# Kernel tuning notes

Measured on AMD Instinct MI355X. Metric: run time of the kernel, lower is better.

Reference implementation:

```python
import jax, jax.numpy as jnp
import numpy as np

D_MODEL = 768
D_INNER = 1536   # expand=2
D_STATE = 16
D_CONV = 4
DT_RANK = 48     # ceil(768/16)
B, T, N = 2, 4, 196


def _rmsnorm(x, w, eps=1e-5):
    var = jnp.mean(x * x, axis=-1, keepdims=True)
    return x * jax.lax.rsqrt(var + eps) * w


def _causal_dwconv(x, w, b):
    # x: (b, l, di), w: (di, k) depthwise, causal left-pad k-1
    xc = jnp.swapaxes(x, 1, 2)  # (b, di, l)
    out = jax.lax.conv_general_dilated(
        xc, w[:, None, :], window_strides=(1,), padding=[(D_CONV - 1, 0)],
        feature_group_count=D_INNER, dimension_numbers=('NCH', 'OIH', 'NCH'))
    return jnp.swapaxes(out + b[None, :, None], 1, 2)


def _selective_scan(u, dt, A, Bm, Cm, Dp):
    # u, dt: (b,l,di); Bm, Cm: (b,l,n); A: (di,n); Dp: (di,)
    dA = jnp.exp(dt[..., None] * A)                    # (b,l,di,n)
    dBu = (dt * u)[..., None] * Bm[:, :, None, :]      # (b,l,di,n)

    def step(h, inp):
        dA_t, dBu_t, C_t = inp
        h = dA_t * h + dBu_t                           # (b,di,n)
        return h, jnp.einsum('bdn,bn->bd', h, C_t)

    h0 = jnp.zeros((u.shape[0], D_INNER, D_STATE), u.dtype)
    _, ys = jax.lax.scan(step, h0, (jnp.swapaxes(dA, 0, 1),
                                    jnp.swapaxes(dBu, 0, 1),
                                    jnp.swapaxes(Cm, 0, 1)))
    return jnp.swapaxes(ys, 0, 1) + u * Dp


def _mamba(x, in_w, cw, cb, xp_w, dt_w, dt_b, A_log, Dp, out_w):
    xz = jnp.einsum('blc,ec->ble', x, in_w)            # (b,l,2*di)
    xb, z = jnp.split(xz, 2, axis=-1)
    xb = jax.nn.silu(_causal_dwconv(xb, cw, cb))
    x_dbl = jnp.einsum('bld,ed->ble', xb, xp_w)        # (b,l,dt_rank+2n)
    dt, Bm, Cm = jnp.split(x_dbl, [DT_RANK, DT_RANK + D_STATE], axis=-1)
    dt = jax.nn.softplus(jnp.einsum('blr,dr->bld', dt, dt_w) + dt_b)
    y = _selective_scan(xb, dt, -jnp.exp(A_log), Bm, Cm, Dp)
    y = y * jax.nn.silu(z)
    return jnp.einsum('bld,cd->blc', y, out_w)


def _block(x, i, norm_w, in_proj_w, conv_w, conv_b, x_proj_w, dt_proj_w,
           dt_proj_b, A_log, D, mix_out_w):
    # residual Mamba block: x + mixer(norm(x)); zero-initialized ssm/conv state
    return x + _mamba(_rmsnorm(x, norm_w[i]), in_proj_w[i], conv_w[i], conv_b[i],
                      x_proj_w[i], dt_proj_w[i], dt_proj_b[i], A_log[i], D[i],
                      mix_out_w[i])


def _bimamba(x, norm_w, in_proj_w, conv_w, conv_b, x_proj_w, dt_proj_w,
             dt_proj_b, A_log, D, mix_out_w, gate_w, gate_b, proj_w, proj_b):
    b, t, n, c = x.shape
    xs = x.reshape(b, t * n, c)
    params = (norm_w, in_proj_w, conv_w, conv_b, x_proj_w, dt_proj_w,
              dt_proj_b, A_log, D, mix_out_w)
    out_f = _block(xs, 0, *params)
    flip_t = lambda y: y.reshape(b, t, n, c)[:, ::-1].reshape(b, t * n, c)
    out_b = flip_t(_block(flip_t(xs), 1, *params))
    gate = jax.nn.sigmoid(
        jnp.einsum('blc,dc->bld', jnp.concatenate([out_f, out_b], -1), gate_w)
        + gate_b)
    out = gate * out_f + (1.0 - gate) * out_b
    out = jnp.einsum('bld,cd->blc', out, proj_w) + proj_b
    return out.reshape(b, t, n, c)


def setup_inputs() -> dict:
    key = jax.random.key(0)
    ks = jax.random.split(key, 12)
    s = 0.02
    a_log = jnp.broadcast_to(
        jnp.log(jnp.arange(1, D_STATE + 1, dtype=jnp.float32)),
        (2, D_INNER, D_STATE)).copy()
    return {
        'x': jax.random.normal(ks[0], (B, T, N, D_MODEL), jnp.float32),
        'norm_w': jnp.ones((2, D_MODEL), jnp.float32),
        'in_proj_w': jax.random.normal(ks[1], (2, 2 * D_INNER, D_MODEL), jnp.float32) * s,
        'conv_w': jax.random.normal(ks[2], (2, D_INNER, D_CONV), jnp.float32) * 0.2,
        'conv_b': jnp.zeros((2, D_INNER), jnp.float32),
        'x_proj_w': jax.random.normal(ks[3], (2, DT_RANK + 2 * D_STATE, D_INNER), jnp.float32) * s,
        'dt_proj_w': jax.random.normal(ks[4], (2, D_INNER, DT_RANK), jnp.float32) * s,
        'dt_proj_b': jax.random.normal(ks[5], (2, D_INNER), jnp.float32) * 0.5 - 4.0,
        'A_log': a_log,
        'D': jnp.ones((2, D_INNER), jnp.float32),
        'mix_out_w': jax.random.normal(ks[6], (2, D_MODEL, D_INNER), jnp.float32) * s,
        'gate_w': jax.random.normal(ks[7], (D_MODEL, 2 * D_MODEL), jnp.float32) * s,
        'gate_b': jnp.zeros((D_MODEL,), jnp.float32),
        'proj_w': jax.random.normal(ks[8], (D_MODEL, D_MODEL), jnp.float32) * s,
        'proj_b': jnp.zeros((D_MODEL,), jnp.float32),
    }


def reference(x, norm_w, in_proj_w, conv_w, conv_b, x_proj_w, dt_proj_w,
              dt_proj_b, A_log, D, mix_out_w, gate_w, gate_b, proj_w, proj_b):
    return _bimamba(x, norm_w, in_proj_w, conv_w, conv_b, x_proj_w, dt_proj_w,
                    dt_proj_b, A_log, D, mix_out_w, gate_w, gate_b, proj_w,
                    proj_b)
```

## Files before the change

### kernel.cpp

```cpp
#include <hip/hip_runtime.h>
#include <cstdint>
#include <cstddef>

#define BB 2
#define TT 4
#define NN 196
#define LL (TT*NN)
#define BLr (BB*LL)
#define CM 768
#define DI 1536
#define DS 16
#define DTR 48
#define XD 80
#define GCH 16
#define LC (LL/GCH)
#define NST (2*BB*DI*DS)

typedef short s16x8 __attribute__((ext_vector_type(8)));
typedef float f32x4 __attribute__((ext_vector_type(4)));

static __device__ __forceinline__ float sigmoidf_(float x) {
  return 1.f / (1.f + __expf(-x));
}
static __device__ __forceinline__ unsigned short f2bf(float f) {
  unsigned int u = __float_as_uint(f);
  unsigned int r = (u + 0x7fffu + ((u >> 16) & 1u)) >> 16;
  return (unsigned short)r;
}
static __device__ __forceinline__ float bf2f(unsigned short u) {
  return __uint_as_float(((unsigned int)u) << 16);
}
static __device__ __forceinline__ float softplusf_(float v) {
  return (v > 20.f) ? v : __logf(1.f + __expf(v));
}
static __device__ __forceinline__ void gload_lds16(const void* g, void* l) {
  __builtin_amdgcn_global_load_lds(
      (const __attribute__((address_space(1))) void*)g,
      (__attribute__((address_space(3))) void*)l, 16, 0, 0);
}

__global__ __launch_bounds__(256) void rmsnorm_k(const float* __restrict__ x,
    const float* __restrict__ nw, unsigned short* __restrict__ xn)
{
  int blk = blockIdx.x;
  int l   = blk % LL;
  int b   = (blk / LL) % BB;
  int dir = blk / (BB*LL);
  int lsrc = l;
  if (dir == 1) { int t = l / NN, n = l % NN; lsrc = (TT-1-t)*NN + n; }
  const float* xp = x + ((size_t)b*LL + lsrc)*CM;
  float s = 0.f;
  for (int c = threadIdx.x; c < CM; c += 256) { float v = xp[c]; s += v*v; }
  #pragma unroll
  for (int off = 32; off > 0; off >>= 1) s += __shfl_down(s, off);
  __shared__ float red[4];
  if ((threadIdx.x & 63) == 0) red[threadIdx.x >> 6] = s;
  __syncthreads();
  float tot = red[0] + red[1] + red[2] + red[3];
  float r = rsqrtf(tot * (1.f/CM) + 1e-5f);
  const float* w = nw + dir*CM;
  unsigned short* o = xn + (size_t)blk*CM;
  for (int c = threadIdx.x; c < CM; c += 256) o[c] = f2bf(xp[c] * r * w[c]);
}

#define S_INW  4718592
#define S_OUTW 2359296
#define S_GATW 1179648
#define S_PRJW 589824
#define S_XPW  245760
#define S_DTW  196608
#define E0 S_INW
#define E1 (E0 + S_OUTW)
#define E2 (E1 + S_GATW)
#define E3 (E2 + S_PRJW)
#define E4 (E3 + S_XPW)
#define E5 (E4 + S_DTW)
__global__ void multicast_k(const float* __restrict__ in_w,
    const float* __restrict__ out_w, const float* __restrict__ gate_w,
    const float* __restrict__ proj_w, const float* __restrict__ xp_w,
    const float* __restrict__ dt_w, unsigned short* __restrict__ dst)
{
  int i = blockIdx.x*256 + threadIdx.x;
  if (i >= E5) return;
  float v;
  if (i < E0)       v = in_w[i];
  else if (i < E1)  v = out_w[i - E0];
  else if (i < E2)  v = gate_w[i - E1];
  else if (i < E3)  v = proj_w[i - E2];
  else if (i < E4)  v = xp_w[i - E3];
  else {
    int j = i - E4, r = j >> 6, c = j & 63;
    v = (c < 48) ? dt_w[r*48 + c] : 0.f;
  }
  dst[i] = f2bf(v);
}

template <int BM, int BN>
__device__ __forceinline__ void gemm_core(
    const unsigned short* __restrict__ A, int lda,
    const unsigned short* __restrict__ W, int ldw,
    int M, int N, int K, int m0, int n0,
    short* As, short* Ws, f32x4 (*acc)[BN/32])
{
  const int tid = threadIdx.x;
  const int wv = tid >> 6, lane = tid & 63;
  const int wm0 = (wv >> 1)*(BM/2), wn0 = (wv & 1)*(BN/2);
  const int lm = lane & 15, g = lane >> 4;
  const int r8 = lane >> 3, ch = lane & 7;
  const int chs = ch ^ r8;
  constexpr int MT = BM/32, NT = BN/32;
  for (int k0 = 0; k0 < K; k0 += 64) {
    #pragma unroll
    for (int e = 0; e < BM/32; ++e) {
      int rb = e*32 + wv*8;
      int gr = m0 + rb + r8; if (gr >= M) gr = M - 1;
      gload_lds16(A + (size_t)gr*lda + k0 + chs*8, &As[rb*64 + lane*8]);
    }
    #pragma unroll
    for (int e = 0; e < BN/32; ++e) {
      int rb = e*32 + wv*8;
      int gn = n0 + rb + r8; if (gn >= N) gn = N - 1;
      gload_lds16(W + (size_t)gn*ldw + k0 + chs*8, &Ws[rb*64 + lane*8]);
    }
    __syncthreads();
    #pragma unroll
    for (int s = 0; s < 2; ++s) {
      s16x8 af[MT], bf[NT];
      #pragma unroll
      for (int i = 0; i < MT; ++i) {
        int R = wm0 + i*16 + lm;
        af[i] = *(const s16x8*)(&As[R*64 + (((s*4 + g) ^ (R & 7))*8)]);
      }
      #pragma unroll
      for (int j = 0; j < NT; ++j) {
        int Rn = wn0 + j*16 + lm;
        bf[j] = *(const s16x8*)(&Ws[Rn*64 + (((s*4 + g) ^ (Rn & 7))*8)]);
      }
      #pragma unroll
      for (int i = 0; i < MT; ++i)
        #pragma unroll
        for (int j = 0; j < NT; ++j)
          acc[i][j] = __builtin_amdgcn_mfma_f32_16x16x32_bf16(af[i], bf[j], acc[i][j], 0, 0, 0);
    }
    __syncthreads();
  }
}

__global__ __launch_bounds__(256, 4) void gemm_in_k(
    const unsigned short* __restrict__ xn, const unsigned short* __restrict__ w,
    unsigned short* __restrict__ xzout)
{
  __shared__ short As[64*64];
  __shared__ short Ws[128*64];
  const int dir = blockIdx.z;
  const unsigned short* A = xn + (size_t)dir*BLr*CM;
  const unsigned short* W = w  + (size_t)dir*2*DI*CM;
  unsigned short* C = xzout + (size_t)dir*BLr*2*DI;
  const int m0 = blockIdx.y*64, n0 = blockIdx.x*128;
  f32x4 acc[2][4];
  #pragma unroll
  for (int i = 0; i < 2; ++i)
    #pragma unroll
    for (int j = 0; j < 4; ++j) acc[i][j] = (f32x4){0.f,0.f,0.f,0.f};
  gemm_core<64,128>(A, CM, W, CM, BLr, 2*DI, CM, m0, n0, As, Ws, acc);
  const int tid = threadIdx.x, wv = tid >> 6, lane = tid & 63;
  const int wm0 = (wv >> 1)*32, wn0 = (wv & 1)*64;
  const int lm = lane & 15, g = lane >> 4;
  #pragma unroll
  for (int i = 0; i < 2; ++i) {
    int row = m0 + wm0 + i*16 + g*4;
    #pragma unroll
    for (int j = 0; j < 4; ++j) {
      int col = n0 + wn0 + j*16 + lm;
      #pragma unroll
      for (int r = 0; r < 4; ++r)
        if (row + r < BLr) C[(size_t)(row + r)*2*DI + col] = f2bf(acc[i][j][r]);
    }
  }
}

__global__ __launch_bounds__(256, 4) void gemm_dt_k(
    const unsigned short* __restrict__ xdblb, const unsigned short* __restrict__ w,
    const float* __restrict__ dtb, float* __restrict__ dtv)
{
  __shared__ short As[64*64];
  __shared__ short Ws[128*64];
  const int dir = blockIdx.z;
  const unsigned short* A = xdblb + (size_t)dir*BLr*64;
  const unsigned short* W = w + (size_t)dir*DI*64;
  float* C = dtv + (size_t)dir*BLr*DI;
  const float* bias = dtb + (size_t)dir*DI;
  const int m0 = blockIdx.y*64, n0 = blockIdx.x*128;
  f32x4 acc[2][4];
  #pragma unroll
  for (int i = 0; i < 2; ++i)
    #pragma unroll
    for (int j = 0; j < 4; ++j) acc[i][j] = (f32x4){0.f,0.f,0.f,0.f};
  gemm_core<64,128>(A, 64, W, 64, BLr, DI, 64, m0, n0, As, Ws, acc);
  const int tid = threadIdx.x, wv = tid >> 6, lane = tid & 63;
  const int wm0 = (wv >> 1)*32, wn0 = (wv & 1)*64;
  const int lm = lane & 15, g = lane >> 4;
  #pragma unroll
  for (int i = 0; i < 2; ++i) {
    int row = m0 + wm0 + i*16 + g*4;
    #pragma unroll
    for (int j = 0; j < 4; ++j) {
      int col = n0 + wn0 + j*16 + lm;
      float bv = bias[col];
      #pragma unroll
      for (int r = 0; r < 4; ++r) {
        if (row + r >= BLr) continue;
        C[(size_t)(row + r)*DI + col] = softplusf_(acc[i][j][r] + bv);
      }
    }
  }
}

__global__ __launch_bounds__(256, 4) void gemm_outp_k(
    const unsigned short* __restrict__ yb, const unsigned short* __restrict__ w,
    const float* __restrict__ x, float* __restrict__ fbuf,
    float* __restrict__ bbuf, unsigned short* __restrict__ cat)
{
  __shared__ short As[64*64];
  __shared__ short Ws[64*64];
  const int dir = blockIdx.z;
  const unsigned short* A = yb + (size_t)dir*BLr*DI;
  const unsigned short* W = w + (size_t)dir*CM*DI;
  const int m0 = blockIdx.y*64, n0 = blockIdx.x*64;
  f32x4 acc[2][2];
  #pragma unroll
  for (int i = 0; i < 2; ++i)
    #pragma unroll
    for (int j = 0; j < 2; ++j) acc[i][j] = (f32x4){0.f,0.f,0.f,0.f};
  gemm_core<64,64>(A, DI, W, DI, BLr, CM, DI, m0, n0, As, Ws, acc);
  const int tid = threadIdx.x, wv = tid >> 6, lane = tid & 63;
  const int wm0 = (wv >> 1)*32, wn0 = (wv & 1)*32;
  const int lm = lane & 15, g = lane >> 4;
  #pragma unroll
  for (int i = 0; i < 2; ++i) {
    int row = m0 + wm0 + i*16 + g*4;
    #pragma unroll
    for (int j = 0; j < 2; ++j) {
      int col = n0 + wn0 + j*16 + lm;
      #pragma unroll
      for (int r = 0; r < 4; ++r) {
        int rr = row + r;
        if (rr >= BLr) continue;
        int rt = rr;
        if (dir == 1) {
          int l = rr % LL, b = rr / LL;
          int t = l / NN, nn = l % NN;
          rt = b*LL + (TT-1-t)*NN + nn;
        }
        float v = x[(size_t)rt*CM + col] + acc[i][j][r];
        if (dir == 0) {
          fbuf[(size_t)rt*CM + col] = v;
          cat[(size_t)rt*(2*CM) + col] = f2bf(v);
        } else {
          bbuf[(size_t)rt*CM + col] = v;
          cat[(size_t)rt*(2*CM) + CM + col] = f2bf(v);
        }
      }
    }
  }
}

__global__ __launch_bounds__(256, 4) void gemm_gate_k(
    const unsigned short* __restrict__ cat, const unsigned short* __restrict__ w,
    const float* __restrict__ gb, const float* __restrict__ fbuf,
    const float* __restrict__ bbuf, unsigned short* __restrict__ mixb)
{
  __shared__ short As[64*64];
  __shared__ short Ws[64*64];
  const int m0 = blockIdx.y*64, n0 = blockIdx.x*64;
  f32x4 acc[2][2];
  #pragma unroll
  for (int i = 0; i < 2; ++i)
    #pragma unroll
    for (int j = 0; j < 2; ++j) acc[i][j] = (f32x4){0.f,0.f,0.f,0.f};
  gemm_core<64,64>(cat, 2*CM, w, 2*CM, BLr, CM, 2*CM, m0, n0, As, Ws, acc);
  const int tid = threadIdx.x, wv = tid >> 6, lane = tid & 63;
  const int wm0 = (wv >> 1)*32, wn0 = (wv & 1)*32;
  const int lm = lane & 15, g = lane >> 4;
  #pragma unroll
  for (int i = 0; i < 2; ++i) {
    int row = m0 + wm0 + i*16 + g*4;
    #pragma unroll
    for (int j = 0; j < 2; ++j) {
      int col = n0 + wn0 + j*16 + lm;
      float bv = gb[col];
      #pragma unroll
      for (int r = 0; r < 4; ++r) {
        int rr = row + r;
        if (rr >= BLr) continue;
        float gg = sigmoidf_(acc[i][j][r] + bv);
        float fv = fbuf[(size_t)rr*CM + col];
        float bo = bbuf[(size_t)rr*CM + col];
        mixb[(size_t)rr*CM + col] = f2bf(gg*fv + (1.f - gg)*bo);
      }
    }
  }
}

__global__ __launch_bounds__(256, 4) void gemm_proj_k(
    const unsigned short* __restrict__ mixb, const unsigned short* __restrict__ w,
    const float* __restrict__ pb, float* __restrict__ out)
{
  __shared__ short As[64*64];
  __shared__ short Ws[64*64];
  const int m0 = blockIdx.y*64, n0 = blockIdx.x*64;
  f32x4 acc[2][2];
  #pragma unroll
  for (int i = 0; i < 2; ++i)
    #pragma unroll
    for (int j = 0; j < 2; ++j) acc[i][j] = (f32x4){0.f,0.f,0.f,0.f};
  gemm_core<64,64>(mixb, CM, w, CM, BLr, CM, CM, m0, n0, As, Ws, acc);
  const int tid = threadIdx.x, wv = tid >> 6, lane = tid & 63;
  const int wm0 = (wv >> 1)*32, wn0 = (wv & 1)*32;
  const int lm = lane & 15, g = lane >> 4;
  #pragma unroll
  for (int i = 0; i < 2; ++i) {
    int row = m0 + wm0 + i*16 + g*4;
    #pragma unroll
    for (int j = 0; j < 2; ++j) {
      int col = n0 + wn0 + j*16 + lm;
      float bv = pb[col];
      #pragma unroll
      for (int r = 0; r < 4; ++r)
        if (row + r < BLr) out[(size_t)(row + r)*CM + col] = acc[i][j][r] + bv;
    }
  }
}

__global__ __launch_bounds__(256, 2) void gemm_xproj(
    const unsigned short* __restrict__ ub, const unsigned short* __restrict__ xpw,
    float* __restrict__ part)
{
  __shared__ short As[128*64];
  __shared__ short Ws[128*64];
  const int ks = blockIdx.x, mt = blockIdx.y, dir = blockIdx.z;
  const unsigned short* A = ub + (size_t)dir*BLr*DI + ks*(DI/8);
  const unsigned short* W = xpw + (size_t)dir*XD*DI + ks*(DI/8);
  const int m0 = mt*128;
  f32x4 acc[4][4];
  #pragma unroll
  for (int i = 0; i < 4; ++i)
    #pragma unroll
    for (int j = 0; j < 4; ++j) acc[i][j] = (f32x4){0.f,0.f,0.f,0.f};
  gemm_core<128,128>(A, DI, W, DI, BLr, XD, DI/8, m0, 0, As, Ws, acc);
  const int tid = threadIdx.x, wv = tid >> 6, lane = tid & 63;
  const int wm0 = (wv >> 1)*64, wn0 = (wv & 1)*64;
  const int lm = lane & 15, g = lane >> 4;
  float* P = part + ((size_t)(dir*8 + ks)*BLr)*XD;
  #pragma unroll
  for (int i = 0; i < 4; ++i) {
    int row = m0 + wm0 + i*16 + g*4;
    #pragma unroll
    for (int j = 0; j < 4; ++j) {
      int col = wn0 + j*16 + lm;
      if (col >= XD) continue;
      #pragma unroll
      for (int r = 0; r < 4; ++r)
        if (row + r < BLr) P[(size_t)(row + r)*XD + col] = acc[i][j][r];
    }
  }
}

__global__ void xreduce_k(const float* __restrict__ part,
    float* __restrict__ xdbl, unsigned short* __restrict__ xdbl_b)
{
  int i = blockIdx.x*256 + threadIdx.x;
  if (i >= 2*BLr*XD) return;
  int c = i % XD;
  int r = i / XD;
  int dir = r / BLr, row = r % BLr;
  float s = 0.f;
  #pragma unroll
  for (int ks = 0; ks < 8; ++ks)
    s += part[((size_t)(dir*8 + ks)*BLr + row)*XD + c];
  xdbl[(size_t)r*XD + c] = s;
  if (c < DTR)      xdbl_b[(size_t)r*64 + c] = f2bf(s);
  else if (c < 64)  xdbl_b[(size_t)r*64 + c] = 0;
}

__global__ __launch_bounds__(256) void conv_silu_k(
    const unsigned short* __restrict__ xz, const float* __restrict__ cw,
    const float* __restrict__ cb, unsigned short* __restrict__ ub)
{
  size_t idx = (size_t)blockIdx.x*256 + threadIdx.x;
  if (idx >= (size_t)2*BLr*DI) return;
  int di  = (int)(idx % DI);
  size_t r = idx / DI;
  int l   = (int)(r % LL);
  int dir = (int)(r / (BB*LL));
  size_t rowbase = r - l;
  const float* w = cw + ((size_t)dir*DI + di)*4;
  float acc = cb[dir*DI + di];
  #pragma unroll
  for (int k = 0; k < 4; ++k) {
    int lp = l - 3 + k;
    if (lp >= 0) acc = fmaf(w[k], bf2f(xz[(rowbase + lp)*(2*DI) + di]), acc);
  }
  float v = acc * sigmoidf_(acc);
  ub[idx] = f2bf(v);
}

__global__ __launch_bounds__(256) void scanA_k(const float* __restrict__ dtv,
    const unsigned short* __restrict__ u, const float* __restrict__ xdbl,
    const float* __restrict__ A_log, float* __restrict__ carry,
    float* __restrict__ Pm)
{
  int bx = blockIdx.x;
  int g = bx & (GCH-1);
  int rest = bx / GCH;
  int dchunk = rest % (DI/64);
  int b   = (rest / (DI/64)) % BB;
  int dir = rest / ((DI/64)*BB);
  int tid = threadIdx.x;
  int dl = tid >> 2, q = tid & 3;
  int d = dchunk*64 + dl;
  size_t rb = ((size_t)dir*BB + b) * LL + (size_t)g*LC;
  const float* dtp = dtv + rb*DI + d;
  const unsigned short* up = u + rb*DI + d;
  const float* xB  = xdbl + rb*XD + DTR + 4*q;
  f32x4 al = *(const f32x4*)(A_log + ((size_t)dir*DI + d)*DS + 4*q);
  float Av[4];
  #pragma unroll
  for (int i = 0; i < 4; ++i) Av[i] = -__expf(al[i]);
  float h[4] = {0.f,0.f,0.f,0.f};
  float S = 0.f;
  float ndt[2], nu[2]; f32x4 nB[2];
  #pragma unroll
  for (int e = 0; e < 2; ++e) {
    ndt[e] = dtp[(size_t)e*DI];
    nu[e]  = bf2f(up[(size_t)e*DI]);
    nB[e]  = *(const f32x4*)(xB + (size_t)e*XD);
  }
  #pragma unroll 2
  for (int j = 0; j < LC; ++j) {
    int s = j & 1;
    float cdt = ndt[s], cu = nu[s];
    f32x4 cB = nB[s];
    int lp = j + 2;
    if (lp < LC) {
      ndt[s] = dtp[(size_t)lp*DI];
      nu[s]  = bf2f(up[(size_t)lp*DI]);
      nB[s]  = *(const f32x4*)(xB + (size_t)lp*XD);
    }
    float du = cdt * cu;
    S += cdt;
    #pragma unroll
    for (int i = 0; i < 4; ++i) {
      float dA = __expf(cdt * Av[i]);
      h[i] = fmaf(dA, h[i], du * cB[i]);
    }
  }
  size_t sid = (((size_t)(dir*BB + b)*DI + d)*DS + 4*q);
  f32x4 hc = {h[0], h[1], h[2], h[3]};
  f32x4 pc = {__expf(Av[0]*S), __expf(Av[1]*S), __expf(Av[2]*S), __expf(Av[3]*S)};
  *(f32x4*)(carry + (size_t)g*NST + sid) = hc;
  *(f32x4*)(Pm    + (size_t)g*NST + sid) = pc;
}

__global__ __launch_bounds__(256) void scanB_k(float* __restrict__ carry,
    const float* __restrict__ Pm)
{
  int sid = blockIdx.x*256 + threadIdx.x;
  float h = 0.f;
  #pragma unroll
  for (int g = 0; g < GCH; ++g) {
    float c = carry[(size_t)g*NST + sid];
    float p = Pm[(size_t)g*NST + sid];
    carry[(size_t)g*NST + sid] = h;
    h = fmaf(p, h, c);
  }
}

__global__ __launch_bounds__(256) void scanC_k(const float* __restrict__ dtv,
    const unsigned short* __restrict__ u, const unsigned short* __restrict__ xz,
    const float* __restrict__ xdbl, const float* __restrict__ A_log,
    const float* __restrict__ Dp, const float* __restrict__ h_in,
    unsigned short* __restrict__ y)
{
  int bx = blockIdx.x;
  int g = bx & (GCH-1);
  int rest = bx / GCH;
  int dchunk = rest % (DI/64);
  int b   = (rest / (DI/64)) % BB;
  int dir = rest / ((DI/64)*BB);
  int tid = threadIdx.x;
  int dl = tid >> 2, q = tid & 3;
  int d = dchunk*64 + dl;
  size_t rb = ((size_t)dir*BB + b) * LL + (size_t)g*LC;
  const float* dtp = dtv + rb*DI + d;
  const unsigned short* up = u + rb*DI + d;
  const unsigned short* zp = xz + rb*(2*DI) + DI + d;
  const float* xB  = xdbl + rb*XD + DTR + 4*q;
  const float* xC  = xB + DS;
  unsigned short* yp = y + rb*DI + d;
  f32x4 al = *(const f32x4*)(A_log + ((size_t)dir*DI + d)*DS + 4*q);
  float Av[4];
  #pragma unroll
  for (int i = 0; i < 4; ++i) Av[i] = -__expf(al[i]);
  float Dd = Dp[dir*DI + d];
  size_t sid = (((size_t)(dir*BB + b)*DI + d)*DS + 4*q);
  f32x4 h4 = *(const f32x4*)(h_in + (size_t)g*NST + sid);
  float h[4] = {h4[0], h4[1], h4[2], h4[3]};
  float ndt[2], nu[2], nz[2]; f32x4 nB[2], nC[2];
  #pragma unroll
  for (int e = 0; e < 2; ++e) {
    ndt[e] = dtp[(size_t)e*DI];
    nu[e]  = bf2f(up[(size_t)e*DI]);
    nz[e]  = bf2f(zp[(size_t)e*(2*DI)]);
    nB[e]  = *(const f32x4*)(xB + (size_t)e*XD);
    nC[e]  = *(const f32x4*)(xC + (size_t)e*XD);
  }
  #pragma unroll 2
  for (int j = 0; j < LC; ++j) {
    int s = j & 1;
    float cdt = ndt[s], cu = nu[s], cz = nz[s];
    f32x4 cB = nB[s], cC = nC[s];
    int lp = j + 2;
    if (lp < LC) {
      ndt[s] = dtp[(size_t)lp*DI];
      nu[s]  = bf2f(up[(size_t)lp*DI]);
      nz[s]  = bf2f(zp[(size_t)lp*(2*DI)]);
      nB[s]  = *(const f32x4*)(xB + (size_t)lp*XD);
      nC[s]  = *(const f32x4*)(xC + (size_t)lp*XD);
    }
    float du = cdt * cu;
    float acc = 0.f;
    #pragma unroll
    for (int i = 0; i < 4; ++i) {
      float dA = __expf(cdt * Av[i]);
      h[i] = fmaf(dA, h[i], du * cB[i]);
      acc = fmaf(h[i], cC[i], acc);
    }
    acc += __shfl_xor(acc, 1);
    acc += __shfl_xor(acc, 2);
    if (q == 0) {
      float yv = (acc + cu * Dd) * (cz * sigmoidf_(cz));
      yp[(size_t)j*DI] = f2bf(yv);
    }
  }
}

extern "C" void kernel_launch(void* const* d_in, const int* in_sizes, int n_in,
                              void* d_out, int out_size, void* d_ws, size_t ws_size,
                              hipStream_t stream)
{
  (void)in_sizes; (void)n_in; (void)out_size; (void)ws_size;
  const float* x      = (const float*)d_in[0];
  const float* norm_w = (const float*)d_in[1];
  const float* in_w   = (const float*)d_in[2];
  const float* conv_w = (const float*)d_in[3];
  const float* conv_b = (const float*)d_in[4];
  const float* xp_w   = (const float*)d_in[5];
  const float* dt_w   = (const float*)d_in[6];
  const float* dt_b   = (const float*)d_in[7];
  const float* A_log  = (const float*)d_in[8];
  const float* Dp     = (const float*)d_in[9];
  const float* out_w  = (const float*)d_in[10];
  const float* gate_w = (const float*)d_in[11];
  const float* gate_b = (const float*)d_in[12];
  const float* proj_w = (const float*)d_in[13];
  const float* proj_b = (const float*)d_in[14];
  float* out = (float*)d_out;
  char* wsb  = (char*)d_ws;

  unsigned short* w_all   = (unsigned short*)(wsb + 0);
  unsigned short* in_w_b  = w_all;
  unsigned short* out_w_b = w_all + E0;
  unsigned short* gate_w_b= w_all + E1;
  unsigned short* proj_w_b= w_all + E2;
  unsigned short* xp_w_b  = w_all + E3;
  unsigned short* dt_w_b  = w_all + E4;
  unsigned short* xz_b = (unsigned short*)(wsb + 18579456);
  unsigned short* ub   = (unsigned short*)(wsb + 37847040);
  float* xdbl  = (float*)(wsb + 57114624);
  float* dtvb  = (float*)(wsb + 58118144);
  unsigned short* y_b = (unsigned short*)(wsb + 77385728);
  unsigned short* tmp = (unsigned short*)(wsb + 87019520);
  float* fbuf  = (float*)(wsb + 96653312);
  float* bbuf  = (float*)(wsb + 101470208);
  unsigned short* cat_b = (unsigned short*)(wsb + 106287104);
  unsigned short* mix_b = (unsigned short*)(wsb + 111104000);

  unsigned short* xn_b   = tmp;
  unsigned short* xdbl_b = tmp;
  float* part  = (float*)(wsb + 0);
  float* carry = (float*)(wsb + 0);
  float* Pmat  = (float*)(wsb + 87019520 + 524288);

  rmsnorm_k<<<2*BLr, 256, 0, stream>>>(x, norm_w, xn_b);
  multicast_k<<<(E5 + 255)/256, 256, 0, stream>>>(
      in_w, out_w, gate_w, proj_w, xp_w, dt_w, w_all);
  gemm_in_k<<<dim3(3072/128, (BLr+63)/64, 2), 256, 0, stream>>>(
      xn_b, in_w_b, xz_b);
  conv_silu_k<<<(int)(((size_t)2*BLr*DI + 255)/256), 256, 0, stream>>>(
      xz_b, conv_w, conv_b, ub);
  gemm_xproj<<<dim3(8, (BLr+127)/128, 2), 256, 0, stream>>>(ub, xp_w_b, part);
  xreduce_k<<<(2*BLr*XD + 255)/256, 256, 0, stream>>>(part, xdbl, xdbl_b);
  gemm_dt_k<<<dim3(DI/128, (BLr+63)/64, 2), 256, 0, stream>>>(
      xdbl_b, dt_w_b, dt_b, dtvb);
  scanA_k<<<2*BB*(DI/64)*GCH, 256, 0, stream>>>(
      dtvb, ub, xdbl, A_log, carry, Pmat);
  scanB_k<<<NST/256, 256, 0, stream>>>(carry, Pmat);
  scanC_k<<<2*BB*(DI/64)*GCH, 256, 0, stream>>>(
      dtvb, ub, xz_b, xdbl, A_log, Dp, carry, y_b);
  gemm_outp_k<<<dim3(CM/64, (BLr+63)/64, 2), 256, 0, stream>>>(
      y_b, out_w_b, x, fbuf, bbuf, cat_b);
  gemm_gate_k<<<dim3(CM/64, (BLr+63)/64, 1), 256, 0, stream>>>(
      cat_b, gate_w_b, gate_b, fbuf, bbuf, mix_b);
  gemm_proj_k<<<dim3(CM/64, (BLr+63)/64, 1), 256, 0, stream>>>(
      mix_b, proj_w_b, proj_b, out);
}
```

Measured before the change: 308.9 us.

## Fuse prep kernels, store dt in bf16, vectorize conv, retune scan chunks and occupancy

```diff
diff --git a/kernel.cpp b/kernel.cpp
--- a/kernel.cpp
+++ b/kernel.cpp
@@ -12,7 +12,7 @@
 #define DS 16
 #define DTR 48
 #define XD 80
-#define GCH 16
+#define GCH 28
 #define LC (LL/GCH)
 #define NST (2*BB*DI*DS)
 
@@ -37,30 +37,6 @@
   __builtin_amdgcn_global_load_lds(
       (const __attribute__((address_space(1))) void*)g,
       (__attribute__((address_space(3))) void*)l, 16, 0, 0);
-}
-
-__global__ __launch_bounds__(256) void rmsnorm_k(const float* __restrict__ x,
-    const float* __restrict__ nw, unsigned short* __restrict__ xn)
-{
-  int blk = blockIdx.x;
-  int l   = blk % LL;
-  int b   = (blk / LL) % BB;
-  int dir = blk / (BB*LL);
-  int lsrc = l;
-  if (dir == 1) { int t = l / NN, n = l % NN; lsrc = (TT-1-t)*NN + n; }
-  const float* xp = x + ((size_t)b*LL + lsrc)*CM;
-  float s = 0.f;
-  for (int c = threadIdx.x; c < CM; c += 256) { float v = xp[c]; s += v*v; }
-  #pragma unroll
-  for (int off = 32; off > 0; off >>= 1) s += __shfl_down(s, off);
-  __shared__ float red[4];
-  if ((threadIdx.x & 63) == 0) red[threadIdx.x >> 6] = s;
-  __syncthreads();
-  float tot = red[0] + red[1] + red[2] + red[3];
-  float r = rsqrtf(tot * (1.f/CM) + 1e-5f);
-  const float* w = nw + dir*CM;
-  unsigned short* o = xn + (size_t)blk*CM;
-  for (int c = threadIdx.x; c < CM; c += 256) o[c] = f2bf(xp[c] * r * w[c]);
 }
 
 #define S_INW  4718592
@@ -75,24 +51,50 @@
 #define E3 (E2 + S_PRJW)
 #define E4 (E3 + S_XPW)
 #define E5 (E4 + S_DTW)
-__global__ void multicast_k(const float* __restrict__ in_w,
-    const float* __restrict__ out_w, const float* __restrict__ gate_w,
-    const float* __restrict__ proj_w, const float* __restrict__ xp_w,
-    const float* __restrict__ dt_w, unsigned short* __restrict__ dst)
-{
-  int i = blockIdx.x*256 + threadIdx.x;
-  if (i >= E5) return;
-  float v;
-  if (i < E0)       v = in_w[i];
-  else if (i < E1)  v = out_w[i - E0];
-  else if (i < E2)  v = gate_w[i - E1];
-  else if (i < E3)  v = proj_w[i - E2];
-  else if (i < E4)  v = xp_w[i - E3];
-  else {
-    int j = i - E4, r = j >> 6, c = j & 63;
-    v = (c < 48) ? dt_w[r*48 + c] : 0.f;
-  }
-  dst[i] = f2bf(v);
+#define MC_BLOCKS ((E5 + 255)/256)
+
+__global__ __launch_bounds__(256) void prep_k(const float* __restrict__ x,
+    const float* __restrict__ nw, unsigned short* __restrict__ xn,
+    const float* __restrict__ in_w, const float* __restrict__ out_w,
+    const float* __restrict__ gate_w, const float* __restrict__ proj_w,
+    const float* __restrict__ xp_w, const float* __restrict__ dt_w,
+    unsigned short* __restrict__ dst)
+{
+  int bx = blockIdx.x;
+  if (bx < 2*BLr) {
+    int l   = bx % LL;
+    int b   = (bx / LL) % BB;
+    int dir = bx / (BB*LL);
+    int lsrc = l;
+    if (dir == 1) { int t = l / NN, n = l % NN; lsrc = (TT-1-t)*NN + n; }
+    const float* xp = x + ((size_t)b*LL + lsrc)*CM;
+    float s = 0.f;
+    for (int c = threadIdx.x; c < CM; c += 256) { float v = xp[c]; s += v*v; }
+    #pragma unroll
+    for (int off = 32; off > 0; off >>= 1) s += __shfl_down(s, off);
+    __shared__ float red[4];
+    if ((threadIdx.x & 63) == 0) red[threadIdx.x >> 6] = s;
+    __syncthreads();
+    float tot = red[0] + red[1] + red[2] + red[3];
+    float r = rsqrtf(tot * (1.f/CM) + 1e-5f);
+    const float* w = nw + dir*CM;
+    unsigned short* o = xn + (size_t)bx*CM;
+    for (int c = threadIdx.x; c < CM; c += 256) o[c] = f2bf(xp[c] * r * w[c]);
+  } else {
+    int i = (bx - 2*BLr)*256 + threadIdx.x;
+    if (i >= E5) return;
+    float v;
+    if (i < E0)       v = in_w[i];
+    else if (i < E1)  v = out_w[i - E0];
+    else if (i < E2)  v = gate_w[i - E1];
+    else if (i < E3)  v = proj_w[i - E2];
+    else if (i < E4)  v = xp_w[i - E3];
+    else {
+      int j = i - E4, r = j >> 6, c = j & 63;
+      v = (c < 48) ? dt_w[r*48 + c] : 0.f;
+    }
+    dst[i] = f2bf(v);
+  }
 }
 
 template <int BM, int BN>
@@ -146,7 +148,7 @@
   }
 }
 
-__global__ __launch_bounds__(256, 4) void gemm_in_k(
+__global__ __launch_bounds__(256, 6) void gemm_in_k(
     const unsigned short* __restrict__ xn, const unsigned short* __restrict__ w,
     unsigned short* __restrict__ xzout)
 {
@@ -179,16 +181,16 @@
   }
 }
 
-__global__ __launch_bounds__(256, 4) void gemm_dt_k(
+__global__ __launch_bounds__(256, 6) void gemm_dt_k(
     const unsigned short* __restrict__ xdblb, const unsigned short* __restrict__ w,
-    const float* __restrict__ dtb, float* __restrict__ dtv)
+    const float* __restrict__ dtb, unsigned short* __restrict__ dtv)
 {
   __shared__ short As[64*64];
   __shared__ short Ws[128*64];
   const int dir = blockIdx.z;
   const unsigned short* A = xdblb + (size_t)dir*BLr*64;
   const unsigned short* W = w + (size_t)dir*DI*64;
-  float* C = dtv + (size_t)dir*BLr*DI;
+  unsigned short* C = dtv + (size_t)dir*BLr*DI;
   const float* bias = dtb + (size_t)dir*DI;
   const int m0 = blockIdx.y*64, n0 = blockIdx.x*128;
   f32x4 acc[2][4];
@@ -210,13 +212,13 @@
       #pragma unroll
       for (int r = 0; r < 4; ++r) {
         if (row + r >= BLr) continue;
-        C[(size_t)(row + r)*DI + col] = softplusf_(acc[i][j][r] + bv);
+        C[(size_t)(row + r)*DI + col] = f2bf(softplusf_(acc[i][j][r] + bv));
       }
     }
   }
 }
 
-__global__ __launch_bounds__(256, 4) void gemm_outp_k(
+__global__ __launch_bounds__(256, 6) void gemm_outp_k(
     const unsigned short* __restrict__ yb, const unsigned short* __restrict__ w,
     const float* __restrict__ x, float* __restrict__ fbuf,
     float* __restrict__ bbuf, unsigned short* __restrict__ cat)
@@ -265,7 +267,7 @@
   }
 }
 
-__global__ __launch_bounds__(256, 4) void gemm_gate_k(
+__global__ __launch_bounds__(256, 6) void gemm_gate_k(
     const unsigned short* __restrict__ cat, const unsigned short* __restrict__ w,
     const float* __restrict__ gb, const float* __restrict__ fbuf,
     const float* __restrict__ bbuf, unsigned short* __restrict__ mixb)
@@ -302,7 +304,7 @@
   }
 }
 
-__global__ __launch_bounds__(256, 4) void gemm_proj_k(
+__global__ __launch_bounds__(256, 6) void gemm_proj_k(
     const unsigned short* __restrict__ mixb, const unsigned short* __restrict__ w,
     const float* __restrict__ pb, float* __restrict__ out)
 {
@@ -332,7 +334,7 @@
   }
 }
 
-__global__ __launch_bounds__(256, 2) void gemm_xproj(
+__global__ __launch_bounds__(256, 4) void gemm_xproj(
     const unsigned short* __restrict__ ub, const unsigned short* __restrict__ xpw,
     float* __restrict__ part)
 {
@@ -387,31 +389,51 @@
     const unsigned short* __restrict__ xz, const float* __restrict__ cw,
     const float* __restrict__ cb, unsigned short* __restrict__ ub)
 {
-  size_t idx = (size_t)blockIdx.x*256 + threadIdx.x;
-  if (idx >= (size_t)2*BLr*DI) return;
-  int di  = (int)(idx % DI);
-  size_t r = idx / DI;
-  int l   = (int)(r % LL);
-  int dir = (int)(r / (BB*LL));
-  size_t rowbase = r - l;
-  const float* w = cw + ((size_t)dir*DI + di)*4;
-  float acc = cb[dir*DI + di];
+  int idx = blockIdx.x*256 + threadIdx.x;
+  if (idx >= 2*BLr*(DI/8)) return;
+  int dg  = idx % (DI/8);
+  int r   = idx / (DI/8);
+  int l   = r % LL;
+  int dir = r / (BB*LL);
+  int di0 = dg*8;
+  size_t rowbase = (size_t)(r - l);
+  const float* wp = cw + ((size_t)dir*DI + di0)*4;
+  float w[32];
+  #pragma unroll
+  for (int i = 0; i < 8; ++i) {
+    f32x4 t = *(const f32x4*)(wp + i*4);
+    w[i*4+0]=t[0]; w[i*4+1]=t[1]; w[i*4+2]=t[2]; w[i*4+3]=t[3];
+  }
+  f32x4 b0 = *(const f32x4*)(cb + dir*DI + di0);
+  f32x4 b1 = *(const f32x4*)(cb + dir*DI + di0 + 4);
+  float acc[8];
+  #pragma unroll
+  for (int c = 0; c < 4; ++c) { acc[c] = b0[c]; acc[4+c] = b1[c]; }
   #pragma unroll
   for (int k = 0; k < 4; ++k) {
     int lp = l - 3 + k;
-    if (lp >= 0) acc = fmaf(w[k], bf2f(xz[(rowbase + lp)*(2*DI) + di]), acc);
-  }
-  float v = acc * sigmoidf_(acc);
-  ub[idx] = f2bf(v);
-}
-
-__global__ __launch_bounds__(256) void scanA_k(const float* __restrict__ dtv,
+    if (lp < 0) continue;
+    s16x8 xv = *(const s16x8*)(xz + (rowbase + lp)*(2*DI) + di0);
+    #pragma unroll
+    for (int c = 0; c < 8; ++c)
+      acc[c] = fmaf(w[c*4+k], bf2f((unsigned short)xv[c]), acc[c]);
+  }
+  s16x8 o;
+  #pragma unroll
+  for (int c = 0; c < 8; ++c) {
+    float v = acc[c] * sigmoidf_(acc[c]);
+    o[c] = (short)f2bf(v);
+  }
+  *(s16x8*)(ub + (size_t)r*DI + di0) = o;
+}
+
+__global__ __launch_bounds__(256) void scanA_k(const unsigned short* __restrict__ dtv,
     const unsigned short* __restrict__ u, const float* __restrict__ xdbl,
     const float* __restrict__ A_log, float* __restrict__ carry,
     float* __restrict__ Pm)
 {
   int bx = blockIdx.x;
-  int g = bx & (GCH-1);
+  int g = bx % GCH;
   int rest = bx / GCH;
   int dchunk = rest % (DI/64);
   int b   = (rest / (DI/64)) % BB;
@@ -420,8 +442,8 @@
   int dl = tid >> 2, q = tid & 3;
   int d = dchunk*64 + dl;
   size_t rb = ((size_t)dir*BB + b) * LL + (size_t)g*LC;
-  const float* dtp = dtv + rb*DI + d;
-  const unsigned short* up = u + rb*DI + d;
+  const unsigned short* dtp = dtv + rb*DI + d;
+  const unsigned short* up  = u + rb*DI + d;
   const float* xB  = xdbl + rb*XD + DTR + 4*q;
   f32x4 al = *(const f32x4*)(A_log + ((size_t)dir*DI + d)*DS + 4*q);
   float Av[4];
@@ -432,7 +454,7 @@
   float ndt[2], nu[2]; f32x4 nB[2];
   #pragma unroll
   for (int e = 0; e < 2; ++e) {
-    ndt[e] = dtp[(size_t)e*DI];
+    ndt[e] = bf2f(dtp[(size_t)e*DI]);
     nu[e]  = bf2f(up[(size_t)e*DI]);
     nB[e]  = *(const f32x4*)(xB + (size_t)e*XD);
   }
@@ -443,7 +465,7 @@
     f32x4 cB = nB[s];
     int lp = j + 2;
     if (lp < LC) {
-      ndt[s] = dtp[(size_t)lp*DI];
+      ndt[s] = bf2f(dtp[(size_t)lp*DI]);
       nu[s]  = bf2f(up[(size_t)lp*DI]);
       nB[s]  = *(const f32x4*)(xB + (size_t)lp*XD);
     }
@@ -476,14 +498,14 @@
   }
 }
 
-__global__ __launch_bounds__(256) void scanC_k(const float* __restrict__ dtv,
+__global__ __launch_bounds__(256) void scanC_k(const unsigned short* __restrict__ dtv,
     const unsigned short* __restrict__ u, const unsigned short* __restrict__ xz,
     const float* __restrict__ xdbl, const float* __restrict__ A_log,
     const float* __restrict__ Dp, const float* __restrict__ h_in,
     unsigned short* __restrict__ y)
 {
   int bx = blockIdx.x;
-  int g = bx & (GCH-1);
+  int g = bx % GCH;
   int rest = bx / GCH;
   int dchunk = rest % (DI/64);
   int b   = (rest / (DI/64)) % BB;
@@ -492,9 +514,9 @@
   int dl = tid >> 2, q = tid & 3;
   int d = dchunk*64 + dl;
   size_t rb = ((size_t)dir*BB + b) * LL + (size_t)g*LC;
-  const float* dtp = dtv + rb*DI + d;
-  const unsigned short* up = u + rb*DI + d;
-  const unsigned short* zp = xz + rb*(2*DI) + DI + d;
+  const unsigned short* dtp = dtv + rb*DI + d;
+  const unsigned short* up  = u + rb*DI + d;
+  const unsigned short* zp  = xz + rb*(2*DI) + DI + d;
   const float* xB  = xdbl + rb*XD + DTR + 4*q;
   const float* xC  = xB + DS;
   unsigned short* yp = y + rb*DI + d;
@@ -509,7 +531,7 @@
   float ndt[2], nu[2], nz[2]; f32x4 nB[2], nC[2];
   #pragma unroll
   for (int e = 0; e < 2; ++e) {
-    ndt[e] = dtp[(size_t)e*DI];
+    ndt[e] = bf2f(dtp[(size_t)e*DI]);
     nu[e]  = bf2f(up[(size_t)e*DI]);
     nz[e]  = bf2f(zp[(size_t)e*(2*DI)]);
     nB[e]  = *(const f32x4*)(xB + (size_t)e*XD);
@@ -522,7 +544,7 @@
     f32x4 cB = nB[s], cC = nC[s];
     int lp = j + 2;
     if (lp < LC) {
-      ndt[s] = dtp[(size_t)lp*DI];
+      ndt[s] = bf2f(dtp[(size_t)lp*DI]);
       nu[s]  = bf2f(up[(size_t)lp*DI]);
       nz[s]  = bf2f(zp[(size_t)lp*(2*DI)]);
       nB[s]  = *(const f32x4*)(xB + (size_t)lp*XD);
@@ -575,39 +597,36 @@
   unsigned short* proj_w_b= w_all + E2;
   unsigned short* xp_w_b  = w_all + E3;
   unsigned short* dt_w_b  = w_all + E4;
-  unsigned short* xz_b = (unsigned short*)(wsb + 18579456);
-  unsigned short* ub   = (unsigned short*)(wsb + 37847040);
-  float* xdbl  = (float*)(wsb + 57114624);
-  float* dtvb  = (float*)(wsb + 58118144);
-  unsigned short* y_b = (unsigned short*)(wsb + 77385728);
-  unsigned short* tmp = (unsigned short*)(wsb + 87019520);
-  float* fbuf  = (float*)(wsb + 96653312);
-  float* bbuf  = (float*)(wsb + 101470208);
-  unsigned short* cat_b = (unsigned short*)(wsb + 106287104);
-  unsigned short* mix_b = (unsigned short*)(wsb + 111104000);
-
-  unsigned short* xn_b   = tmp;
-  unsigned short* xdbl_b = tmp;
-  float* part  = (float*)(wsb + 0);
-  float* carry = (float*)(wsb + 0);
-  float* Pmat  = (float*)(wsb + 87019520 + 524288);
-
-  rmsnorm_k<<<2*BLr, 256, 0, stream>>>(x, norm_w, xn_b);
-  multicast_k<<<(E5 + 255)/256, 256, 0, stream>>>(
-      in_w, out_w, gate_w, proj_w, xp_w, dt_w, w_all);
+  unsigned short* xz_b   = (unsigned short*)(wsb + 18579456);
+  unsigned short* ub     = (unsigned short*)(wsb + 37847040);
+  float*          xdbl   = (float*)(wsb + 47480832);
+  unsigned short* xdbl_b = (unsigned short*)(wsb + 48484352);
+  unsigned short* dtv_b  = (unsigned short*)(wsb + 48885760);
+  unsigned short* y_b    = (unsigned short*)(wsb + 58519552);
+  float*          fbuf   = (float*)(wsb + 68153344);
+  float*          bbuf   = (float*)(wsb + 72970240);
+  unsigned short* cat_b  = (unsigned short*)(wsb + 77787136);
+  unsigned short* mix_b  = (unsigned short*)(wsb + 82604032);
+  float*          part   = (float*)(wsb + 85012480);
+  float*          carry  = (float*)(wsb + 93040640);
+  float*          Pmat   = (float*)(wsb + 104050688);
+  unsigned short* xn_b   = (unsigned short*)(wsb + 115060736);
+
+  prep_k<<<2*BLr + MC_BLOCKS, 256, 0, stream>>>(
+      x, norm_w, xn_b, in_w, out_w, gate_w, proj_w, xp_w, dt_w, w_all);
   gemm_in_k<<<dim3(3072/128, (BLr+63)/64, 2), 256, 0, stream>>>(
       xn_b, in_w_b, xz_b);
-  conv_silu_k<<<(int)(((size_t)2*BLr*DI + 255)/256), 256, 0, stream>>>(
+  conv_silu_k<<<(2*BLr*(DI/8) + 255)/256, 256, 0, stream>>>(
       xz_b, conv_w, conv_b, ub);
   gemm_xproj<<<dim3(8, (BLr+127)/128, 2), 256, 0, stream>>>(ub, xp_w_b, part);
   xreduce_k<<<(2*BLr*XD + 255)/256, 256, 0, stream>>>(part, xdbl, xdbl_b);
   gemm_dt_k<<<dim3(DI/128, (BLr+63)/64, 2), 256, 0, stream>>>(
-      xdbl_b, dt_w_b, dt_b, dtvb);
+      xdbl_b, dt_w_b, dt_b, dtv_b);
   scanA_k<<<2*BB*(DI/64)*GCH, 256, 0, stream>>>(
-      dtvb, ub, xdbl, A_log, carry, Pmat);
+      dtv_b, ub, xdbl, A_log, carry, Pmat);
   scanB_k<<<NST/256, 256, 0, stream>>>(carry, Pmat);
   scanC_k<<<2*BB*(DI/64)*GCH, 256, 0, stream>>>(
-      dtvb, ub, xz_b, xdbl, A_log, Dp, carry, y_b);
+      dtv_b, ub, xz_b, xdbl, A_log, Dp, carry, y_b);
   gemm_outp_k<<<dim3(CM/64, (BLr+63)/64, 2), 256, 0, stream>>>(
       y_b, out_w_b, x, fbuf, bbuf, cat_b);
   gemm_gate_k<<<dim3(CM/64, (BLr+63)/64, 1), 256, 0, stream>>>(
```

After: 342.6 us. +10.9%, slower.
